# Performance work log

Measured on AMD Instinct MI355X. Metric: run time of the kernel, lower is better.

The kernel has to match this reference:

```python
import jax, jax.numpy as jnp
import numpy as np
import math

NUM_HEADS = 16
WINDOW = 128  # telephone/sliding-window size: attend to self + previous WINDOW-1 tokens
EPS = 1e-6


def setup_inputs() -> dict:
    key = jax.random.key(0)
    k1, k2, k3, k4 = jax.random.split(key, 4)
    B, S, D = 4, 4096, 1024
    x = jax.random.normal(k1, (B, S, D), dtype=jnp.float32)
    g = jnp.ones((D,), dtype=jnp.float32)  # RMSNorm weight
    Wqkv = jax.random.normal(k2, (D, 3 * D), dtype=jnp.float32) * 0.02
    Wo = jax.random.normal(k3, (D, D), dtype=jnp.float32) * 0.02
    return {"x": x, "g": g, "Wqkv": Wqkv, "Wo": Wo}


def _telephone_block(x, g, Wqkv, Wo):
    B, S, D = x.shape
    H, dh, W = NUM_HEADS, D // NUM_HEADS, WINDOW
    nb = S // W  # number of key/query blocks

    # pre-RMSNorm
    xn = x * jax.lax.rsqrt(jnp.mean(x * x, axis=-1, keepdims=True) + EPS) * g

    # fused QKV projection
    qkv = xn @ Wqkv  # [B,S,3D]
    q, k, v = jnp.split(qkv, 3, axis=-1)

    def split_heads(t):
        # [B,S,D] -> [B,H,nb,W,dh]
        return t.reshape(B, nb, W, H, dh).transpose(0, 3, 1, 2, 4)

    q, k, v = split_heads(q), split_heads(k), split_heads(v)

    def shift_prev(t):
        # previous block of keys/values (zeros for block 0, masked below)
        return jnp.pad(t[:, :, :-1], ((0, 0), (0, 0), (1, 0), (0, 0), (0, 0)))

    k_ext = jnp.concatenate([shift_prev(k), k], axis=3)  # [B,H,nb,2W,dh]
    v_ext = jnp.concatenate([shift_prev(v), v], axis=3)

    scale = 1.0 / math.sqrt(dh)
    scores = jnp.einsum('bhnqd,bhnkd->bhnqk', q, k_ext) * scale  # [B,H,nb,W,2W]

    # sliding-window causal mask within the [prev-block, cur-block] key span.
    # query local pos i in [0,W); key extended pos j in [0,2W) maps to offset j-W.
    i = jnp.arange(W)[:, None]
    j = jnp.arange(2 * W)[None, :]
    base = (j > i) & (j <= i + W)          # last W tokens incl. self
    first = base & (j >= W)                # block 0 has no previous block
    blk0 = (jnp.arange(nb) == 0)[:, None, None]
    mask = jnp.where(blk0, first[None], base[None])  # [nb,W,2W]

    scores = jnp.where(mask[None, None], scores, jnp.finfo(scores.dtype).min)
    p = jax.nn.softmax(scores, axis=-1)
    o = jnp.einsum('bhnqk,bhnkd->bhnqd', p, v_ext)   # [B,H,nb,W,dh]
    o = o.transpose(0, 2, 3, 1, 4).reshape(B, S, D)
    h = o @ Wo
    return x + h  # residual


def reference(x, g, Wqkv, Wo):
    return _telephone_block(x, g, Wqkv, Wo)
```

## Files before the change

### kernel.cpp

```cpp
#include <hip/hip_runtime.h>
#include <hip/hip_bf16.h>


typedef __attribute__((ext_vector_type(8))) short s8v;
typedef __attribute__((ext_vector_type(4))) float f4v;

#define MFMA_BF16(A, B, C) __builtin_amdgcn_mfma_f32_16x16x32_bf16((A), (B), (C), 0, 0, 0)

static __device__ __forceinline__ void gload_lds16(const void* g, void* l) {
    __builtin_amdgcn_global_load_lds((const __attribute__((address_space(1))) void*)g,
                                     (__attribute__((address_space(3))) void*)l, 16, 0, 0);
}

static __device__ __forceinline__ unsigned short f2bf(float f) {
    return __builtin_bit_cast(unsigned short, __float2bfloat16(f));
}

__global__ __launch_bounds__(256) void transpose_cast_kernel(const float* __restrict__ Wqkv,
                                                             unsigned short* __restrict__ WqkvT,
                                                             const float* __restrict__ Wo,
                                                             unsigned short* __restrict__ WoT) {
    const int K = 1024;
    int nb1 = (K >> 5) * (3072 >> 5);
    const float* in;
    unsigned short* out;
    int N, bidx;
    if (blockIdx.x < (unsigned)nb1) {
        in = Wqkv; out = WqkvT; N = 3072; bidx = blockIdx.x;
    } else {
        in = Wo; out = WoT; N = 1024; bidx = blockIdx.x - nb1;
    }
    __shared__ float tile[32][33];
    int nbk = K >> 5;
    int bk = bidx % nbk;
    int bn = bidx / nbk;
    int tx = threadIdx.x & 31, ty = threadIdx.x >> 5;
#pragma unroll
    for (int i = 0; i < 4; i++) {
        int r = ty + i * 8;
        tile[r][tx] = in[(size_t)(bk * 32 + r) * N + bn * 32 + tx];
    }
    __syncthreads();
#pragma unroll
    for (int i = 0; i < 4; i++) {
        int r = ty + i * 8;
        out[(size_t)(bn * 32 + r) * K + bk * 32 + tx] = f2bf(tile[tx][r]);
    }
}

__global__ __launch_bounds__(256) void rmsnorm_kernel(const float* __restrict__ x,
                                                      const float* __restrict__ g,
                                                      unsigned short* __restrict__ xn) {
    const int D = 1024;
    int row = blockIdx.x;
    int t = threadIdx.x;
    float4 v = ((const float4*)(x + (size_t)row * D))[t];
    float ss = v.x * v.x + v.y * v.y + v.z * v.z + v.w * v.w;
#pragma unroll
    for (int off = 32; off >= 1; off >>= 1) ss += __shfl_xor(ss, off, 64);
    __shared__ float partials[4];
    if ((t & 63) == 0) partials[t >> 6] = ss;
    __syncthreads();
    float tot = partials[0] + partials[1] + partials[2] + partials[3];
    float scale = rsqrtf(tot * (1.0f / D) + 1e-6f);
    float4 gv = ((const float4*)g)[t];
    ushort4 o;
    o.x = f2bf(v.x * scale * gv.x);
    o.y = f2bf(v.y * scale * gv.y);
    o.z = f2bf(v.z * scale * gv.z);
    o.w = f2bf(v.w * scale * gv.w);
    ((ushort4*)xn)[(size_t)row * (D / 4) + t] = o;
}

template <int MODE>
__global__ __launch_bounds__(512, 2) void gemm256_kernel(const unsigned short* __restrict__ A,
                                                         const unsigned short* __restrict__ Bt,
                                                         unsigned short* __restrict__ Cb,
                                                         float* __restrict__ Cf,
                                                         const float* __restrict__ resid,
                                                         int M, int N, int K) {
    __shared__ __align__(16) char lds_s[131072];

    const int nbn = N >> 8;
    const int nwg = (M >> 8) * nbn;
    int bid = blockIdx.x;
    int cpx = nwg >> 3;
    int wg = (bid & 7) * cpx + (bid >> 3);
    int bm = wg / nbn, bn = wg % nbn;

    int tid = threadIdx.x, lane = tid & 63, w = tid >> 6;
    int wm = w >> 2, wn = w & 3;
    int hl = lane >> 4, ll = lane & 15;

    const unsigned short* Ab = A + (size_t)bm * 256 * K;
    const unsigned short* Bb = Bt + (size_t)bn * 256 * K;

    int srow = lane >> 3;
    int scol = ((lane & 7) ^ srow) * 8;

    int c0 = (hl * 16) ^ ((ll & 7) * 16);
    const char* ldsA0 = lds_s + wm * 16384 + ll * 128 + c0;
    const char* ldsA1 = lds_s + wm * 16384 + ll * 128 + (c0 ^ 64);
    const char* ldsB0 = lds_s + 32768 + (wn >> 1) * 16384 + ((wn & 1) * 64 + ll) * 128 + c0;
    const char* ldsB1 = lds_s + 32768 + (wn >> 1) * 16384 + ((wn & 1) * 64 + ll) * 128 + (c0 ^ 64);

    const int NT = K >> 6;

    f4v acc[8][4] = {};
    s8v bfr[4][2];

#define STAGE(t_, isB_, h_) do {                                                          \
        int te_ = (t_) < NT ? (t_) : (t_)-NT;                                             \
        const unsigned short* g_ = ((isB_) ? Bb : Ab)                                     \
            + (size_t)((h_)*128 + srow) * K + te_ * 64 + scol;                            \
        char* l_ = lds_s + (((t_)&1) * 65536 + (isB_)*32768 + (h_)*16384);                \
        gload_lds16(g_ + (size_t)(w * 8) * K, l_ + w * 1024);                             \
        gload_lds16(g_ + (size_t)(64 + w * 8) * K, l_ + 8192 + w * 1024);                 \
    } while (0)

#define PHASE(buf_, p4_, st_, sb_, sh_, dv_) do {                                         \
        s8v a0k0 = *(const s8v*)(ldsA0 + (buf_)*65536 + (2 * (p4_)) * 2048);              \
        s8v a0k1 = *(const s8v*)(ldsA1 + (buf_)*65536 + (2 * (p4_)) * 2048);              \
        s8v a1k0 = *(const s8v*)(ldsA0 + (buf_)*65536 + (2 * (p4_) + 1) * 2048);          \
        s8v a1k1 = *(const s8v*)(ldsA1 + (buf_)*65536 + (2 * (p4_) + 1) * 2048);          \
        if ((p4_) == 0) {                                                                 \
            _Pragma("unroll") for (int n = 0; n < 4; n++) {                               \
                bfr[n][0] = *(const s8v*)(ldsB0 + (buf_)*65536 + n * 2048);               \
                bfr[n][1] = *(const s8v*)(ldsB1 + (buf_)*65536 + n * 2048);               \
            }                                                                             \
        }                                                                                 \
        STAGE(st_, sb_, sh_);                                                             \
        if (dv_) asm volatile("s_waitcnt vmcnt(4)" ::: "memory");                         \
        asm volatile("s_barrier" ::: "memory");                                           \
        asm volatile("s_waitcnt lgkmcnt(0)" ::: "memory");                                \
        __builtin_amdgcn_s_setprio(1);                                                    \
        _Pragma("unroll") for (int n = 0; n < 4; n++) {                                   \
            acc[2 * (p4_)][n] = MFMA_BF16(a0k0, bfr[n][0], acc[2 * (p4_)][n]);            \
            acc[2 * (p4_)][n] = MFMA_BF16(a0k1, bfr[n][1], acc[2 * (p4_)][n]);            \
            acc[2 * (p4_) + 1][n] = MFMA_BF16(a1k0, bfr[n][0], acc[2 * (p4_) + 1][n]);    \
            acc[2 * (p4_) + 1][n] = MFMA_BF16(a1k1, bfr[n][1], acc[2 * (p4_) + 1][n]);    \
        }                                                                                 \
        __builtin_amdgcn_s_setprio(0);                                                    \
        asm volatile("s_barrier" ::: "memory");                                           \
    } while (0)

    STAGE(0, 0, 0); STAGE(0, 0, 1); STAGE(0, 1, 0); STAGE(0, 1, 1);
    STAGE(1, 1, 0); STAGE(1, 1, 1);
    asm volatile("s_waitcnt vmcnt(4)" ::: "memory");
    asm volatile("s_barrier" ::: "memory");

    for (int i = 0; i < NT / 2; i++) {
        int t1 = 2 * i + 1;
        PHASE(0, 0, t1, 0, 0, 0);
        PHASE(0, 1, t1, 0, 1, 0);
        PHASE(0, 2, t1 + 1, 1, 0, 0);
        PHASE(0, 3, t1 + 1, 1, 1, 1);
        PHASE(1, 0, t1 + 1, 0, 0, 0);
        PHASE(1, 1, t1 + 1, 0, 1, 0);
        PHASE(1, 2, t1 + 2, 1, 0, 0);
        PHASE(1, 3, t1 + 2, 1, 1, 1);
    }
#undef PHASE
#undef STAGE

    int crow0 = bm * 256 + wm * 128;
    int ccol0 = bn * 256 + wn * 64;
#pragma unroll
    for (int m = 0; m < 8; m++) {
#pragma unroll
        for (int r = 0; r < 4; r++) {
            int row = crow0 + m * 16 + hl * 4 + r;
#pragma unroll
            for (int n = 0; n < 4; n++) {
                int col = ccol0 + n * 16 + ll;
                float val = acc[m][n][r];
                if (MODE == 0) {
                    Cb[(size_t)row * N + col] = f2bf(val);
                } else {
                    size_t idx = (size_t)row * N + col;
                    Cf[idx] = resid[idx] + val;
                }
            }
        }
    }
}

__global__ __launch_bounds__(256, 3) void attn_kernel(const unsigned short* __restrict__ qkv,
                                                      unsigned short* __restrict__ obuf) {
    constexpr int S = 4096, D = 1024, H = 16, W = 128, NB = 32;
    constexpr int TD = 3 * D;
    constexpr int PS = 40;

    __shared__ __align__(16) char smem[44032];
    unsigned short* KV = (unsigned short*)smem;

    int bid = blockIdx.x;
    int blk = bid % NB;
    int h = (bid / NB) % H;
    int b = bid / (NB * H);

    int tid = threadIdx.x, lane = tid & 63, w = tid >> 6;
    int hl = lane >> 4, ll = lane & 15;
    unsigned short* Ps = (unsigned short*)(smem + 33792) + w * 32 * PS;

    int kbase = blk * W - W;
    size_t rowbase = (size_t)(b * S);

    {
        int lr = lane >> 3;
        int scb = ((lane & 7) ^ lr) * 16;
#pragma unroll
        for (int r = 0; r < 8; r++) {
            int row = r * 32 + w * 8 + lr;
            int s = kbase + row;
            s = s < 0 ? 0 : s;
            const char* src = (const char*)(qkv + (rowbase + s) * TD + D + h * 64) + scb;
            char* dst = smem + (size_t)(r * 32 + w * 8) * 128 + lane * 16;
            gload_lds16(src, dst);
        }
    }

    s8v qf[2][2];
    {
        const unsigned short* qb = qkv + (rowbase + blk * W + w * 32) * TD + h * 64;
#pragma unroll
        for (int mf = 0; mf < 2; mf++)
#pragma unroll
            for (int ks = 0; ks < 2; ks++)
                qf[mf][ks] = *(const s8v*)(qb + (size_t)(mf * 16 + ll) * TD + ks * 32 + hl * 8);
    }

    s8v vreg[8];
    {
        int k0 = w * 64 + (lane >> 3) * 8;
        int d0 = (lane & 7) * 8;
#pragma unroll
        for (int it = 0; it < 8; it++) {
            int s = kbase + k0 + it;
            s = s < 0 ? 0 : s;
            vreg[it] = *(const s8v*)(qkv + (rowbase + s) * TD + 2 * D + h * 64 + d0);
        }
    }
    __syncthreads();

    f4v sc[2][9] = {};
    int g0 = w * 2;
    __builtin_amdgcn_s_setprio(1);
#pragma unroll
    for (int gi = 0; gi < 10; gi++) {
#pragma unroll
        for (int ks = 0; ks < 2; ks++) {
            int row = (g0 + gi) * 16 + ll;
            s8v kf = *(const s8v*)(smem + (size_t)row * 128 +
                                   (((unsigned)(ks * 64 + hl * 16)) ^ ((ll & 7) << 4)));
            if (gi < 9) sc[0][gi] = MFMA_BF16(qf[0][ks], kf, sc[0][gi]);
            if (gi > 0) sc[1][gi - 1] = MFMA_BF16(qf[1][ks], kf, sc[1][gi - 1]);
        }
    }
    __builtin_amdgcn_s_setprio(0);

    float linv[2][4];
#pragma unroll
    for (int mf = 0; mf < 2; mf++) {
#pragma unroll
        for (int r = 0; r < 4; r++) {
            int ip = hl * 4 + r;
            float mx = -1e30f;
#pragma unroll
            for (int nf = 0; nf < 9; nf++) {
                bool ok = (nf > 0 || ll > ip) && (nf < 8 || ll <= ip) &&
                          (blk > 0 || (g0 + mf + nf) >= 8);
                float sval = ok ? sc[mf][nf][r] * 0.125f : -1e30f;
                sc[mf][nf][r] = sval;
                mx = fmaxf(mx, sval);
            }
#pragma unroll
            for (int off = 1; off < 16; off <<= 1) mx = fmaxf(mx, __shfl_xor(mx, off, 64));
            float sum = 0.f;
#pragma unroll
            for (int nf = 0; nf < 9; nf++) {
                float p = __expf(sc[mf][nf][r] - mx);
                sc[mf][nf][r] = p;
                sum += p;
            }
#pragma unroll
            for (int off = 1; off < 16; off <<= 1) sum += __shfl_xor(sum, off, 64);
            linv[mf][r] = 1.f / sum;
        }
    }

    __syncthreads();

    {
        int k0 = w * 64 + (lane >> 3) * 8;
        int d0 = (lane & 7) * 8;
#pragma unroll
        for (int e = 0; e < 8; e++) {
            int d = d0 + e;
            s8v tmp;
#pragma unroll
            for (int i = 0; i < 8; i++) tmp[i] = vreg[i][e];
            *(s8v*)(KV + d * 264 + (k0 ^ (((d >> 3) & 7) << 3))) = tmp;
        }
    }
    __syncthreads();

    f4v o[2][4] = {};
#pragma unroll
    for (int c = 0; c < 5; c++) {
#pragma unroll
        for (int mf = 0; mf < 2; mf++) {
#pragma unroll
            for (int j16 = 0; j16 < 2; j16++) {
                int nf = c * 2 + j16 - mf;
                int nfc = nf < 0 ? 0 : (nf > 8 ? 8 : nf);
#pragma unroll
                for (int r = 0; r < 4; r++) {
                    float val = (nf >= 0 && nf < 9) ? sc[mf][nfc][r] : 0.f;
                    Ps[(mf * 16 + hl * 4 + r) * PS + j16 * 16 + ll] = f2bf(val);
                }
            }
        }
        asm volatile("s_waitcnt lgkmcnt(0)" ::: "memory");
        s8v pa[2];
        pa[0] = *(const s8v*)(Ps + ll * PS + hl * 8);
        pa[1] = *(const s8v*)(Ps + (16 + ll) * PS + hl * 8);
        int cb = (w + c) * 32;
        __builtin_amdgcn_s_setprio(1);
#pragma unroll
        for (int nd = 0; nd < 4; nd++) {
            int d = nd * 16 + ll;
            int kk = (cb + hl * 8) ^ (((d >> 3) & 7) << 3);
            s8v vb = *(const s8v*)(KV + d * 264 + kk);
            o[0][nd] = MFMA_BF16(pa[0], vb, o[0][nd]);
            o[1][nd] = MFMA_BF16(pa[1], vb, o[1][nd]);
        }
        __builtin_amdgcn_s_setprio(0);
    }

    unsigned short* ob = obuf + (rowbase + blk * W + w * 32) * D + h * 64;
#pragma unroll
    for (int mf = 0; mf < 2; mf++)
#pragma unroll
        for (int r = 0; r < 4; r++) {
            int row = mf * 16 + hl * 4 + r;
#pragma unroll
            for (int nd = 0; nd < 4; nd++)
                ob[(size_t)row * D + nd * 16 + ll] = f2bf(o[mf][nd][r] * linv[mf][r]);
        }
}

extern "C" void kernel_launch(void* const* d_in, const int* in_sizes, int n_in,
                              void* d_out, int out_size, void* d_ws, size_t ws_size,
                              hipStream_t stream) {
    const float* x = (const float*)d_in[0];
    const float* g = (const float*)d_in[1];
    const float* Wqkv = (const float*)d_in[2];
    const float* Wo = (const float*)d_in[3];
    float* out = (float*)d_out;

    const int S = 4096, D = 1024, B = 4;
    const int M = B * S;
    const int N3 = 3 * D;

    char* ws = (char*)d_ws;
    unsigned short* WqkvT = (unsigned short*)ws;
    unsigned short* WoT = (unsigned short*)(ws + 6291456);
    unsigned short* xn = (unsigned short*)(ws + 8388608);
    unsigned short* qkv = (unsigned short*)(ws + 41943040);

    transpose_cast_kernel<<<dim3((D / 32) * (N3 / 32) + (D / 32) * (D / 32)), dim3(256), 0,
                            stream>>>(Wqkv, WqkvT, Wo, WoT);
    rmsnorm_kernel<<<dim3(M), dim3(256), 0, stream>>>(x, g, xn);
    gemm256_kernel<0><<<dim3((M / 256) * (N3 / 256)), dim3(512), 0, stream>>>(
        xn, WqkvT, qkv, nullptr, nullptr, M, N3, D);
    attn_kernel<<<dim3(B * 16 * (S / 128)), dim3(256), 0, stream>>>(qkv, xn);
    gemm256_kernel<1><<<dim3((M / 256) * (D / 256)), dim3(512), 0, stream>>>(
        xn, WoT, nullptr, out, x, M, D, D);
}
```

Baseline: 207.7 us.

## Switch GEMMs to 32x32x16 MFMA tiles and merge prep kernels

Replaces the 16x16x32 bf16 MFMA inner loop of both GEMMs with 32x32x16 MFMAs. This reorganizes the LDS swizzled fragment addressing, the accumulator layout and the epilogue indexing. The aim is fewer LDS fragment reads per FLOP and higher MFMA throughput per instruction. Separately, the RMSNorm and weight transpose/cast kernels are fused into a single launch to save one kernel launch. The risk is that the new swizzle causes LDS bank conflicts or that the fragment mapping is subtly wrong.

```diff
diff --git a/kernel.cpp b/kernel.cpp
--- a/kernel.cpp
+++ b/kernel.cpp
@@ -4,8 +4,10 @@
 
 typedef __attribute__((ext_vector_type(8))) short s8v;
 typedef __attribute__((ext_vector_type(4))) float f4v;
+typedef __attribute__((ext_vector_type(16))) float f16v;
 
 #define MFMA_BF16(A, B, C) __builtin_amdgcn_mfma_f32_16x16x32_bf16((A), (B), (C), 0, 0, 0)
+#define MFMA32_BF16(A, B, C) __builtin_amdgcn_mfma_f32_32x32x16_bf16((A), (B), (C), 0, 0, 0)
 
 static __device__ __forceinline__ void gload_lds16(const void* g, void* l) {
     __builtin_amdgcn_global_load_lds((const __attribute__((address_space(1))) void*)g,
@@ -16,60 +18,61 @@
     return __builtin_bit_cast(unsigned short, __float2bfloat16(f));
 }
 
-__global__ __launch_bounds__(256) void transpose_cast_kernel(const float* __restrict__ Wqkv,
-                                                             unsigned short* __restrict__ WqkvT,
-                                                             const float* __restrict__ Wo,
-                                                             unsigned short* __restrict__ WoT) {
-    const int K = 1024;
-    int nb1 = (K >> 5) * (3072 >> 5);
-    const float* in;
-    unsigned short* out;
-    int N, bidx;
-    if (blockIdx.x < (unsigned)nb1) {
-        in = Wqkv; out = WqkvT; N = 3072; bidx = blockIdx.x;
+__global__ __launch_bounds__(256) void prep_kernel(const float* __restrict__ x,
+                                                   const float* __restrict__ g,
+                                                   unsigned short* __restrict__ xn,
+                                                   const float* __restrict__ Wqkv,
+                                                   unsigned short* __restrict__ WqkvT,
+                                                   const float* __restrict__ Wo,
+                                                   unsigned short* __restrict__ WoT) {
+    const int D = 1024, M = 16384;
+    if (blockIdx.x < (unsigned)M) {
+        int row = blockIdx.x;
+        int t = threadIdx.x;
+        float4 v = ((const float4*)(x + (size_t)row * D))[t];
+        float ss = v.x * v.x + v.y * v.y + v.z * v.z + v.w * v.w;
+#pragma unroll
+        for (int off = 32; off >= 1; off >>= 1) ss += __shfl_xor(ss, off, 64);
+        __shared__ float partials[4];
+        if ((t & 63) == 0) partials[t >> 6] = ss;
+        __syncthreads();
+        float tot = partials[0] + partials[1] + partials[2] + partials[3];
+        float scale = rsqrtf(tot * (1.0f / D) + 1e-6f);
+        float4 gv = ((const float4*)g)[t];
+        ushort4 o;
+        o.x = f2bf(v.x * scale * gv.x);
+        o.y = f2bf(v.y * scale * gv.y);
+        o.z = f2bf(v.z * scale * gv.z);
+        o.w = f2bf(v.w * scale * gv.w);
+        ((ushort4*)xn)[(size_t)row * (D / 4) + t] = o;
     } else {
-        in = Wo; out = WoT; N = 1024; bidx = blockIdx.x - nb1;
-    }
-    __shared__ float tile[32][33];
-    int nbk = K >> 5;
-    int bk = bidx % nbk;
-    int bn = bidx / nbk;
-    int tx = threadIdx.x & 31, ty = threadIdx.x >> 5;
-#pragma unroll
-    for (int i = 0; i < 4; i++) {
-        int r = ty + i * 8;
-        tile[r][tx] = in[(size_t)(bk * 32 + r) * N + bn * 32 + tx];
-    }
-    __syncthreads();
-#pragma unroll
-    for (int i = 0; i < 4; i++) {
-        int r = ty + i * 8;
-        out[(size_t)(bn * 32 + r) * K + bk * 32 + tx] = f2bf(tile[tx][r]);
-    }
-}
-
-__global__ __launch_bounds__(256) void rmsnorm_kernel(const float* __restrict__ x,
-                                                      const float* __restrict__ g,
-                                                      unsigned short* __restrict__ xn) {
-    const int D = 1024;
-    int row = blockIdx.x;
-    int t = threadIdx.x;
-    float4 v = ((const float4*)(x + (size_t)row * D))[t];
-    float ss = v.x * v.x + v.y * v.y + v.z * v.z + v.w * v.w;
-#pragma unroll
-    for (int off = 32; off >= 1; off >>= 1) ss += __shfl_xor(ss, off, 64);
-    __shared__ float partials[4];
-    if ((t & 63) == 0) partials[t >> 6] = ss;
-    __syncthreads();
-    float tot = partials[0] + partials[1] + partials[2] + partials[3];
-    float scale = rsqrtf(tot * (1.0f / D) + 1e-6f);
-    float4 gv = ((const float4*)g)[t];
-    ushort4 o;
-    o.x = f2bf(v.x * scale * gv.x);
-    o.y = f2bf(v.y * scale * gv.y);
-    o.z = f2bf(v.z * scale * gv.z);
-    o.w = f2bf(v.w * scale * gv.w);
-    ((ushort4*)xn)[(size_t)row * (D / 4) + t] = o;
+        int nb1 = (D >> 5) * (3072 >> 5);
+        int bidx = blockIdx.x - M;
+        const float* in;
+        unsigned short* out;
+        int N;
+        if (bidx < nb1) {
+            in = Wqkv; out = WqkvT; N = 3072;
+        } else {
+            in = Wo; out = WoT; N = 1024; bidx -= nb1;
+        }
+        __shared__ float tile[32][33];
+        int nbk = D >> 5;
+        int bk = bidx % nbk;
+        int bn = bidx / nbk;
+        int tx = threadIdx.x & 31, ty = threadIdx.x >> 5;
+#pragma unroll
+        for (int i = 0; i < 4; i++) {
+            int r = ty + i * 8;
+            tile[r][tx] = in[(size_t)(bk * 32 + r) * N + bn * 32 + tx];
+        }
+        __syncthreads();
+#pragma unroll
+        for (int i = 0; i < 4; i++) {
+            int r = ty + i * 8;
+            out[(size_t)(bn * 32 + r) * D + bk * 32 + tx] = f2bf(tile[tx][r]);
+        }
+    }
 }
 
 template <int MODE>
@@ -90,7 +93,7 @@
 
     int tid = threadIdx.x, lane = tid & 63, w = tid >> 6;
     int wm = w >> 2, wn = w & 3;
-    int hl = lane >> 4, ll = lane & 15;
+    int l31 = lane & 31, hi = lane >> 5, l7 = lane & 7;
 
     const unsigned short* Ab = A + (size_t)bm * 256 * K;
     const unsigned short* Bb = Bt + (size_t)bn * 256 * K;
@@ -98,16 +101,23 @@
     int srow = lane >> 3;
     int scol = ((lane & 7) ^ srow) * 8;
 
-    int c0 = (hl * 16) ^ ((ll & 7) * 16);
-    const char* ldsA0 = lds_s + wm * 16384 + ll * 128 + c0;
-    const char* ldsA1 = lds_s + wm * 16384 + ll * 128 + (c0 ^ 64);
-    const char* ldsB0 = lds_s + 32768 + (wn >> 1) * 16384 + ((wn & 1) * 64 + ll) * 128 + c0;
-    const char* ldsB1 = lds_s + 32768 + (wn >> 1) * 16384 + ((wn & 1) * 64 + ll) * 128 + (c0 ^ 64);
+    int sw0 = ((0 | hi) ^ l7) << 4;
+    int sw1 = ((2 | hi) ^ l7) << 4;
+    int sw2 = ((4 | hi) ^ l7) << 4;
+    int sw3 = ((6 | hi) ^ l7) << 4;
+    const char* ldsA_0 = lds_s + wm * 16384 + l31 * 128 + sw0;
+    const char* ldsA_1 = lds_s + wm * 16384 + l31 * 128 + sw1;
+    const char* ldsA_2 = lds_s + wm * 16384 + l31 * 128 + sw2;
+    const char* ldsA_3 = lds_s + wm * 16384 + l31 * 128 + sw3;
+    const char* ldsB_0 = lds_s + 32768 + (wn * 64 + l31) * 128 + sw0;
+    const char* ldsB_1 = lds_s + 32768 + (wn * 64 + l31) * 128 + sw1;
+    const char* ldsB_2 = lds_s + 32768 + (wn * 64 + l31) * 128 + sw2;
+    const char* ldsB_3 = lds_s + 32768 + (wn * 64 + l31) * 128 + sw3;
 
     const int NT = K >> 6;
 
-    f4v acc[8][4] = {};
-    s8v bfr[4][2];
+    f16v acc[4][2] = {};
+    s8v bfr[2][4];
 
 #define STAGE(t_, isB_, h_) do {                                                          \
         int te_ = (t_) < NT ? (t_) : (t_)-NT;                                             \
@@ -119,14 +129,16 @@
     } while (0)
 
 #define PHASE(buf_, p4_, st_, sb_, sh_, dv_) do {                                         \
-        s8v a0k0 = *(const s8v*)(ldsA0 + (buf_)*65536 + (2 * (p4_)) * 2048);              \
-        s8v a0k1 = *(const s8v*)(ldsA1 + (buf_)*65536 + (2 * (p4_)) * 2048);              \
-        s8v a1k0 = *(const s8v*)(ldsA0 + (buf_)*65536 + (2 * (p4_) + 1) * 2048);          \
-        s8v a1k1 = *(const s8v*)(ldsA1 + (buf_)*65536 + (2 * (p4_) + 1) * 2048);          \
+        s8v a0 = *(const s8v*)(ldsA_0 + (buf_)*65536 + (p4_)*4096);                       \
+        s8v a1 = *(const s8v*)(ldsA_1 + (buf_)*65536 + (p4_)*4096);                       \
+        s8v a2 = *(const s8v*)(ldsA_2 + (buf_)*65536 + (p4_)*4096);                       \
+        s8v a3 = *(const s8v*)(ldsA_3 + (buf_)*65536 + (p4_)*4096);                       \
         if ((p4_) == 0) {                                                                 \
-            _Pragma("unroll") for (int n = 0; n < 4; n++) {                               \
-                bfr[n][0] = *(const s8v*)(ldsB0 + (buf_)*65536 + n * 2048);               \
-                bfr[n][1] = *(const s8v*)(ldsB1 + (buf_)*65536 + n * 2048);               \
+            _Pragma("unroll") for (int nf = 0; nf < 2; nf++) {                            \
+                bfr[nf][0] = *(const s8v*)(ldsB_0 + (buf_)*65536 + nf * 4096);            \
+                bfr[nf][1] = *(const s8v*)(ldsB_1 + (buf_)*65536 + nf * 4096);            \
+                bfr[nf][2] = *(const s8v*)(ldsB_2 + (buf_)*65536 + nf * 4096);            \
+                bfr[nf][3] = *(const s8v*)(ldsB_3 + (buf_)*65536 + nf * 4096);            \
             }                                                                             \
         }                                                                                 \
         STAGE(st_, sb_, sh_);                                                             \
@@ -134,12 +146,14 @@
         asm volatile("s_barrier" ::: "memory");                                           \
         asm volatile("s_waitcnt lgkmcnt(0)" ::: "memory");                                \
         __builtin_amdgcn_s_setprio(1);                                                    \
-        _Pragma("unroll") for (int n = 0; n < 4; n++) {                                   \
-            acc[2 * (p4_)][n] = MFMA_BF16(a0k0, bfr[n][0], acc[2 * (p4_)][n]);            \
-            acc[2 * (p4_)][n] = MFMA_BF16(a0k1, bfr[n][1], acc[2 * (p4_)][n]);            \
-            acc[2 * (p4_) + 1][n] = MFMA_BF16(a1k0, bfr[n][0], acc[2 * (p4_) + 1][n]);    \
-            acc[2 * (p4_) + 1][n] = MFMA_BF16(a1k1, bfr[n][1], acc[2 * (p4_) + 1][n]);    \
-        }                                                                                 \
+        acc[p4_][0] = MFMA32_BF16(a0, bfr[0][0], acc[p4_][0]);                            \
+        acc[p4_][1] = MFMA32_BF16(a0, bfr[1][0], acc[p4_][1]);                            \
+        acc[p4_][0] = MFMA32_BF16(a1, bfr[0][1], acc[p4_][0]);                            \
+        acc[p4_][1] = MFMA32_BF16(a1, bfr[1][1], acc[p4_][1]);                            \
+        acc[p4_][0] = MFMA32_BF16(a2, bfr[0][2], acc[p4_][0]);                            \
+        acc[p4_][1] = MFMA32_BF16(a2, bfr[1][2], acc[p4_][1]);                            \
+        acc[p4_][0] = MFMA32_BF16(a3, bfr[0][3], acc[p4_][0]);                            \
+        acc[p4_][1] = MFMA32_BF16(a3, bfr[1][3], acc[p4_][1]);                            \
         __builtin_amdgcn_s_setprio(0);                                                    \
         asm volatile("s_barrier" ::: "memory");                                           \
     } while (0)
@@ -163,17 +177,17 @@
 #undef PHASE
 #undef STAGE
 
-    int crow0 = bm * 256 + wm * 128;
-    int ccol0 = bn * 256 + wn * 64;
-#pragma unroll
-    for (int m = 0; m < 8; m++) {
-#pragma unroll
-        for (int r = 0; r < 4; r++) {
-            int row = crow0 + m * 16 + hl * 4 + r;
-#pragma unroll
-            for (int n = 0; n < 4; n++) {
-                int col = ccol0 + n * 16 + ll;
-                float val = acc[m][n][r];
+    int crow0 = bm * 256 + wm * 128 + hi * 4;
+    int ccol0 = bn * 256 + wn * 64 + l31;
+#pragma unroll
+    for (int m = 0; m < 4; m++) {
+#pragma unroll
+        for (int n = 0; n < 2; n++) {
+#pragma unroll
+            for (int reg = 0; reg < 16; reg++) {
+                int row = crow0 + m * 32 + (reg & 3) + ((reg >> 2) << 3);
+                int col = ccol0 + n * 32;
+                float val = acc[m][n][reg];
                 if (MODE == 0) {
                     Cb[(size_t)row * N + col] = f2bf(val);
                 } else {
@@ -369,9 +383,8 @@
     unsigned short* xn = (unsigned short*)(ws + 8388608);
     unsigned short* qkv = (unsigned short*)(ws + 41943040);
 
-    transpose_cast_kernel<<<dim3((D / 32) * (N3 / 32) + (D / 32) * (D / 32)), dim3(256), 0,
-                            stream>>>(Wqkv, WqkvT, Wo, WoT);
-    rmsnorm_kernel<<<dim3(M), dim3(256), 0, stream>>>(x, g, xn);
+    int prep_grid = M + (D / 32) * (N3 / 32) + (D / 32) * (D / 32);
+    prep_kernel<<<dim3(prep_grid), dim3(256), 0, stream>>>(x, g, xn, Wqkv, WqkvT, Wo, WoT);
     gemm256_kernel<0><<<dim3((M / 256) * (N3 / 256)), dim3(512), 0, stream>>>(
         xn, WqkvT, qkv, nullptr, nullptr, M, N3, D);
     attn_kernel<<<dim3(B * 16 * (S / 128)), dim3(256), 0, stream>>>(qkv, xn);
```

Measured after the change: 239.3 us. 1.15x slower.
